# Kernel optimization log

Measured on AMD Instinct MI355X. Metric: run time of the kernel, lower is better.

## Reference

```python
import jax, jax.numpy as jnp
import numpy as np

N = 512   # particles
T = 128   # timesteps
V_L = 3.4
V_0 = 4.2
GAMMA = 0.9
ALPHA = 0.15
BETA = 15.0
E_CRIT_INV = 2e-5
F_STD = 0.05
G_STD = 0.02
NU = 1.0 / (G_STD * float(np.sqrt(2.0 * np.pi)))
CUR_MIN = 0.0
CUR_MAX = 1.0


def voc(soc):
    # open-circuit voltage model
    return (V_L + (V_0 - V_L) * jnp.exp(GAMMA * (soc - 1.0))
            + ALPHA * V_L * (soc - 1.0)
            + (1.0 - ALPHA) * V_L * (jnp.exp(-BETA) - jnp.exp(-BETA * jnp.sqrt(soc))))


def mlp(x, w1, b1, w2, b2, w3, b3):
    h = jax.nn.sigmoid(x @ w1 + b1)
    h = jax.nn.sigmoid(h @ w2 + b2)
    return h @ w3 + b3


def setup_inputs() -> dict:
    key = jax.random.key(0)
    ks = jax.random.split(key, 11)
    soc_init = jax.random.uniform(ks[0], (N, 1), jnp.float32, 0.6, 1.0)
    current = jax.random.uniform(ks[1], (1, T), jnp.float32)
    voltage_measured = 3.4 + 0.8 * jax.random.uniform(ks[2], (1, T), jnp.float32)
    noise = jax.random.normal(ks[3], (T, N, 1), jnp.float32)
    u = jax.random.uniform(ks[4], (T,), jnp.float32)
    w1 = jax.random.normal(ks[5], (2, 1024), jnp.float32) / np.float32(np.sqrt(2.0))
    b1 = jnp.zeros((1024,), jnp.float32)
    w2 = jax.random.normal(ks[6], (1024, 512), jnp.float32) / np.float32(np.sqrt(1024.0))
    b2 = jnp.zeros((512,), jnp.float32)
    w3 = jax.random.normal(ks[7], (512, 1), jnp.float32) / np.float32(np.sqrt(512.0))
    b3 = jnp.zeros((1,), jnp.float32)
    return {"soc_init": soc_init, "current": current, "voltage_measured": voltage_measured,
            "noise": noise, "u": u, "w1": w1, "b1": b1, "w2": w2, "b2": b2, "w3": w3, "b3": b3}


def reference(soc_init, current, voltage_measured, noise, u, w1, b1, w2, b2, w3, b3):
    n = soc_init.shape[0]
    # pre-loop step: V at t=0 conditions
    I0 = current[0, 0] * jnp.ones_like(soc_init)
    sI0 = (I0 - CUR_MIN) / (CUR_MAX - CUR_MIN)
    Z0 = mlp(jnp.concatenate([soc_init, sI0], axis=1), w1, b1, w2, b2, w3, b3)
    V0 = voc(soc_init) - I0 * Z0

    log_n = jnp.log(jnp.float32(n))

    def step(carry, xs):
        soc, I, V = carry
        cur_t, vmeas_t, noise_t, u_t = xs
        # state propagation with process noise, then clamp to (0, 1]
        soc = soc - I * V * E_CRIT_INV + F_STD * noise_t
        soc = jnp.where(soc > 1.0, 1.0, jnp.where(soc < 0.0, 1e-10, soc))
        I = cur_t * jnp.ones_like(soc)
        sI = (I - CUR_MIN) / (CUR_MAX - CUR_MIN)
        Z = mlp(jnp.concatenate([soc, sI], axis=1), w1, b1, w2, b2, w3, b3)  # [N,1]
        V = voc(soc) - I * Z                                                 # [N,1]
        # importance weights / step loss (logsumexp trick as in source)
        logW = jnp.log(jnp.float32(NU)) - 0.5 * jnp.square((V - vmeas_t) / G_STD)
        step_loss = jax.nn.logsumexp(logW) - log_n
        # systematic resampling on normalized weights
        wn = jax.nn.softmax(logW[:, 0])          # normalized weights [N]
        cum = jnp.cumsum(wn)
        pos = (jnp.arange(n, dtype=jnp.float32) + u_t) / jnp.float32(n)
        idx = jnp.clip(jnp.searchsorted(cum, pos), 0, n - 1)
        soc_r = soc[idx]
        return (soc_r, I, V), (V[:, 0], soc_r[:, 0], step_loss)

    xs = (current[0], voltage_measured[0], noise, u)
    _, (v_hist, s_hist, losses) = jax.lax.scan(step, (soc_init, I0, V0), xs)
    loss = jnp.sum(losses)
    voltage = v_hist.T    # [N, T]
    soc_hist = s_hist.T   # [N, T]
    return loss, voltage, soc_hist
```

## Files before the change

kernel.cpp:

```cpp
#include <hip/hip_runtime.h>
#include <hip/hip_bf16.h>
#include <math.h>

#define N_PART 512
#define T_STEPS 128
#define G_NODES 33
#define TAB2D (G_NODES * G_NODES)
#define ROWS (T_STEPS * G_NODES)
#define V_L 3.4f
#define V_0 4.2f
#define GAMMA 0.9f
#define ALPHA 0.15f
#define BETA 15.0f
#define E_CRIT_INV 2e-5f
#define F_STD 0.05f
#define G_STD 0.02f

#define LBAR() asm volatile("s_waitcnt lgkmcnt(0)\n\ts_barrier" ::: "memory")

__device__ __forceinline__ float sigmoid_jax(float x) {
    float e = expf(-fabsf(x));
    float num = (x >= 0.f) ? 1.f : e;
    return num / (1.f + e);
}

__device__ __forceinline__ float vocf(float s) {
    float sm1 = s - 1.f;
    return V_L + (V_0 - V_L) * expf(GAMMA * sm1)
         + (ALPHA * V_L) * sm1
         + (1.f - ALPHA) * V_L * (expf(-BETA) - expf(-BETA * sqrtf(s)));
}

template <int R>
__device__ __forceinline__ int dpp_ror(int v) {
    return __builtin_amdgcn_update_dpp(0, v, 0x120 | R, 0xf, 0xf, false);
}
template <int S>
__device__ __forceinline__ int dpp_shr(int v) {
    return __builtin_amdgcn_update_dpp(0, v, 0x110 | S, 0xf, 0xf, true);
}
__device__ __forceinline__ float fror(float v, float o) { return o; }

__device__ __forceinline__ float wave_max_f(float v) {
    v = fmaxf(v, __int_as_float(dpp_ror<1>(__float_as_int(v))));
    v = fmaxf(v, __int_as_float(dpp_ror<2>(__float_as_int(v))));
    v = fmaxf(v, __int_as_float(dpp_ror<4>(__float_as_int(v))));
    v = fmaxf(v, __int_as_float(dpp_ror<8>(__float_as_int(v))));
    int iv = __float_as_int(v);
    v = fmaxf(v, __int_as_float(__builtin_amdgcn_update_dpp(iv, iv, 0x142, 0xf, 0xf, false)));
    iv = __float_as_int(v);
    v = fmaxf(v, __int_as_float(__builtin_amdgcn_update_dpp(iv, iv, 0x143, 0xf, 0xf, false)));
    return __int_as_float(__builtin_amdgcn_readlane(__float_as_int(v), 63));
}

__device__ __forceinline__ int wave_max_i(int v) {
    v = max(v, dpp_ror<1>(v));
    v = max(v, dpp_ror<2>(v));
    v = max(v, dpp_ror<4>(v));
    v = max(v, dpp_ror<8>(v));
    v = max(v, __builtin_amdgcn_update_dpp(v, v, 0x142, 0xf, 0xf, false));
    v = max(v, __builtin_amdgcn_update_dpp(v, v, 0x143, 0xf, 0xf, false));
    return __builtin_amdgcn_readlane(v, 63);
}

__device__ __forceinline__ float wave_scan_add(float v, int lane) {
    v += __int_as_float(dpp_shr<1>(__float_as_int(v)));
    v += __int_as_float(dpp_shr<2>(__float_as_int(v)));
    v += __int_as_float(dpp_shr<4>(__float_as_int(v)));
    v += __int_as_float(dpp_shr<8>(__float_as_int(v)));
    float s15 = __int_as_float(__builtin_amdgcn_readlane(__float_as_int(v), 15));
    float s31 = __int_as_float(__builtin_amdgcn_readlane(__float_as_int(v), 31));
    float s47 = __int_as_float(__builtin_amdgcn_readlane(__float_as_int(v), 47));
    int row = lane >> 4;
    if (row >= 1) v += s15;
    if (row >= 2) v += s31;
    if (row >= 3) v += s47;
    return v;
}

__device__ __forceinline__ int wave_scanmax_i(int v, int lane) {
    v = max(v, dpp_shr<1>(v));
    v = max(v, dpp_shr<2>(v));
    v = max(v, dpp_shr<4>(v));
    v = max(v, dpp_shr<8>(v));
    int r15 = __builtin_amdgcn_readlane(v, 15);
    int r31 = __builtin_amdgcn_readlane(v, 31);
    int r47 = __builtin_amdgcn_readlane(v, 47);
    int row = lane >> 4;
    if (row >= 1) v = max(v, r15);
    if (row >= 2) v = max(v, r31);
    if (row >= 3) v = max(v, r47);
    return v;
}

#define BKT 32
__global__ __launch_bounds__(256) void k_tab(
    const float* __restrict__ w1, const float* __restrict__ b1,
    const float* __restrict__ w2, const float* __restrict__ b2,
    const float* __restrict__ w3, float* __restrict__ zpart)
{
    const int tid = threadIdx.x;
    const int rowblk = blockIdx.x >> 1;
    const int colhalf = blockIdx.x & 1;
    const int r0 = rowblk * 8;
    const int cbase = colhalf * 256;

    __shared__ float As[8][BKT + 1];
    __shared__ float Bs[BKT][256];
    __shared__ float srow[8], irow[8];

    if (tid < 8) {
        int r = r0 + tid;
        r = r > (TAB2D - 1) ? (TAB2D - 1) : r;
        int si = r / G_NODES;
        int ii = r - si * G_NODES;
        srow[tid] = (float)si * (1.0f / 32.0f);
        irow[tid] = (float)ii * (1.0f / 32.0f);
    }
    __syncthreads();

    const int rg = tid >> 5;
    const int ct = tid & 31;
    float acc[8];
    #pragma unroll
    for (int b = 0; b < 8; ++b) acc[b] = 0.f;

    for (int kk = 0; kk < 1024; kk += BKT) {
        {
            int kc = kk + ct;
            float pre = srow[rg] * w1[kc] + irow[rg] * w1[1024 + kc] + b1[kc];
            As[rg][ct] = sigmoid_jax(pre);
        }
        #pragma unroll
        for (int jj = 0; jj < 8; ++jj) {
            int vi = tid + jj * 256;
            int k = vi >> 6, c4 = vi & 63;
            *(float4*)&Bs[k][c4 * 4] = *(const float4*)&w2[(kk + k) * 512 + cbase + c4 * 4];
        }
        __syncthreads();
        #pragma unroll
        for (int k = 0; k < BKT; ++k) {
            float a = As[rg][k];
            float bq[8];
            *(float4*)&bq[0] = *(const float4*)&Bs[k][ct * 4];
            *(float4*)&bq[4] = *(const float4*)&Bs[k][ct * 4 + 128];
            #pragma unroll
            for (int q = 0; q < 8; ++q) acc[q] += a * bq[q];
        }
        __syncthreads();
    }

    float b2r[8], w3r[8];
    *(float4*)&b2r[0] = *(const float4*)&b2[cbase + ct * 4];
    *(float4*)&b2r[4] = *(const float4*)&b2[cbase + ct * 4 + 128];
    *(float4*)&w3r[0] = *(const float4*)&w3[cbase + ct * 4];
    *(float4*)&w3r[4] = *(const float4*)&w3[cbase + ct * 4 + 128];
    float zp = 0.f;
    #pragma unroll
    for (int q = 0; q < 8; ++q)
        zp += w3r[q] * sigmoid_jax(acc[q] + b2r[q]);
    #pragma unroll
    for (int mm = 1; mm < 32; mm <<= 1) zp += __shfl_xor(zp, mm);
    if (ct == 0 && (r0 + rg) < TAB2D)
        zpart[colhalf * TAB2D + r0 + rg] = zp;
}

__device__ __forceinline__ float interp_tab(const float* __restrict__ row, int stride, float s) {
    float x = s * 32.0f;
    int j = (int)floorf(x);
    j = j < 0 ? 0 : (j > 31 ? 31 : j);
    int st = j - 1;
    st = st < 0 ? 0 : (st > 29 ? 29 : st);
    float uu = x - (float)st;
    float um0 = uu, um1 = uu - 1.f, um2 = uu - 2.f, um3 = uu - 3.f;
    float w0 = um1 * um2 * um3 * (-1.f / 6.f);
    float w1 = um0 * um2 * um3 * (0.5f);
    float w2 = um0 * um1 * um3 * (-0.5f);
    float w3 = um0 * um1 * um2 * (1.f / 6.f);
    return w0 * row[st * stride] + w1 * row[(st + 1) * stride]
         + w2 * row[(st + 2) * stride] + w3 * row[(st + 3) * stride];
}

__device__ __forceinline__ int count_le(float C, float u) {
    int h = (int)floorf(C - u);
    h = h < -1 ? -1 : (h > 511 ? 511 : h);
    h += (int)((h < 511) && (((float)(h + 1) + u) <= C));
    h += (int)((h < 511) && (((float)(h + 1) + u) <= C));
    h -= (int)((h >= 0) && (((float)h + u) > C));
    h -= (int)((h >= 0) && (((float)h + u) > C));
    return h + 1;
}

__global__ __launch_bounds__(512, 1) void k_seq(
    const float* __restrict__ zpart, const float* __restrict__ soc_init,
    const float* __restrict__ current, const float* __restrict__ vmeas,
    const float* __restrict__ u, const float* __restrict__ noise,
    const float* __restrict__ b3, float* __restrict__ vbuf,
    float* __restrict__ sbuf, float* __restrict__ out)
{
    const int tid = threadIdx.x;
    const int lane = tid & 63;
    const int wid = tid >> 6;

    __shared__ float zt[ROWS];
    __shared__ float zt2d[TAB2D];
    __shared__ float socs[2][512];
    __shared__ int marker[512];
    __shared__ float cur_s[128], vm_s[128], u_s[128];
    __shared__ float redM[8], redT[8];

    float bb3 = b3[0];
    for (int j = tid; j < TAB2D; j += 512) zt2d[j] = zpart[j] + zpart[TAB2D + j] + bb3;
    if (tid < 128) { cur_s[tid] = current[tid]; vm_s[tid] = vmeas[tid]; u_s[tid] = u[tid]; }
    marker[tid] = 0;
    __syncthreads();

    for (int idx = tid; idx < ROWS; idx += 512) {
        int t = idx / G_NODES;
        int g = idx - t * G_NODES;
        zt[idx] = interp_tab(&zt2d[g * G_NODES], 1, cur_s[t]);
    }
    __syncthreads();

    float soc = soc_init[tid];
    float Iprev = cur_s[0];
    float V = vocf(soc) - Iprev * interp_tab(&zt[0], 1, soc);
    float loss_acc = 0.f;
    const float LOG_NU = logf(19.947114020071635f);
    const float LOG_N = logf(512.f);

    float nz_cur = noise[tid];

    for (int t = 0; t < T_STEPS; ++t) {
        int tn = (t + 1 < T_STEPS) ? t + 1 : t;
        float nz_next = noise[tn * 512 + tid];

        soc = soc - Iprev * V * E_CRIT_INV + F_STD * nz_cur;
        soc = soc > 1.f ? 1.f : (soc < 0.f ? 1e-10f : soc);
        socs[t & 1][tid] = soc;

        float I = cur_s[t];
        V = vocf(soc) - I * interp_tab(&zt[t * G_NODES], 1, soc);
        float d = (V - vm_s[t]) * (1.f / G_STD);
        float lw = LOG_NU - 0.5f * d * d;

        float m = wave_max_f(lw);
        float e = expf(lw - m);
        float incl = wave_scan_add(e, lane);
        if (lane == 63) { redM[wid] = m; redT[wid] = incl; }
        LBAR();

        float rm = redM[lane & 7];
        float rt = redT[lane & 7];
        float M = rm;
        M = fmaxf(M, __int_as_float(dpp_ror<1>(__float_as_int(M))));
        M = fmaxf(M, __int_as_float(dpp_ror<2>(__float_as_int(M))));
        M = fmaxf(M, __int_as_float(dpp_ror<4>(__float_as_int(M))));
        M = fmaxf(M, __int_as_float(dpp_ror<8>(__float_as_int(M))));
        float fw = expf(rm - M);
        float term = rt * fw;
        float sc = term;
        sc += __int_as_float(dpp_shr<1>(__float_as_int(sc)));
        sc += __int_as_float(dpp_shr<2>(__float_as_int(sc)));
        sc += __int_as_float(dpp_shr<4>(__float_as_int(sc)));
        float S = __int_as_float(__builtin_amdgcn_readlane(__float_as_int(sc), 7));
        float off = 0.f;
        if (wid > 0) off = __int_as_float(__builtin_amdgcn_readlane(__float_as_int(sc), wid - 1));
        float fw_own = __int_as_float(__builtin_amdgcn_readlane(__float_as_int(fw), wid));
        loss_acc += M + logf(S) - LOG_N;

        float C = 512.f * ((off + incl * fw_own) / S);
        int hi = count_le(C, u_s[t]);
        if (hi < 512) atomicMax(&marker[hi], (t << 10) | (tid + 1));
        LBAR();

        int pm = 0;
        for (int w = 0; w < wid; ++w) pm = max(pm, marker[w * 64 + lane]);
        pm = wave_max_i(pm);
        int v = wave_scanmax_i(marker[tid], lane);
        int sv = max(v, pm);
        int owner = ((sv >> 10) == t) ? (sv & 1023) : 0;
        owner = owner > 511 ? 511 : owner;
        float socr = socs[t & 1][owner];

        vbuf[t * 512 + tid] = V;
        sbuf[t * 512 + tid] = socr;
        soc = socr;
        Iprev = I;
        nz_cur = nz_next;
    }
    if (tid == 0) out[0] = loss_acc;
}

__global__ __launch_bounds__(256) void k_fin(
    const float* __restrict__ vbuf, const float* __restrict__ sbuf,
    float* __restrict__ out)
{
    __shared__ float tile[32][33];
    int tz = blockIdx.z;
    int t0 = blockIdx.x * 32;
    int i0 = blockIdx.y * 32;
    const float* src = tz ? sbuf : vbuf;
    float* dst = out + 1 + tz * (N_PART * T_STEPS);
    int tx = threadIdx.x & 31, ty = threadIdx.x >> 5;
    #pragma unroll
    for (int m2 = 0; m2 < 4; ++m2)
        tile[ty + 8 * m2][tx] = src[(t0 + ty + 8 * m2) * 512 + i0 + tx];
    __syncthreads();
    #pragma unroll
    for (int m2 = 0; m2 < 4; ++m2)
        dst[(i0 + ty + 8 * m2) * 128 + t0 + tx] = tile[tx][ty + 8 * m2];
}

extern "C" void kernel_launch(void* const* d_in, const int* in_sizes, int n_in,
                              void* d_out, int out_size, void* d_ws, size_t ws_size,
                              hipStream_t stream)
{
    const float* soc_init = (const float*)d_in[0];
    const float* current  = (const float*)d_in[1];
    const float* vmeas    = (const float*)d_in[2];
    const float* noise    = (const float*)d_in[3];
    const float* u        = (const float*)d_in[4];
    const float* w1 = (const float*)d_in[5];
    const float* b1 = (const float*)d_in[6];
    const float* w2 = (const float*)d_in[7];
    const float* b2 = (const float*)d_in[8];
    const float* w3 = (const float*)d_in[9];
    const float* b3 = (const float*)d_in[10];
    float* out = (float*)d_out;
    float* ws  = (float*)d_ws;

    float* zpart = ws;
    float* vbuf  = ws + 2 * TAB2D;
    float* sbuf  = vbuf + N_PART * T_STEPS;

    k_tab<<<274, 256, 0, stream>>>(w1, b1, w2, b2, w3, zpart);
    k_seq<<<1, 512, 0, stream>>>(zpart, soc_init, current, vmeas, u, noise, b3,
                                 vbuf, sbuf, out);
    k_fin<<<dim3(4, 16, 2), 256, 0, stream>>>(vbuf, sbuf, out);
}
```

Before: 286.2 us.

## Precompute per-timestep voltage tables on a finer grid to shorten the sequential loop

Before the sequential loop, a per-timestep voltage table V(t, soc) is built on a 193-point soc grid by combining the open-circuit voltage with the interpolated MLP output. Each step then needs only one cubic interpolation from this table instead of evaluating vocf (several exp and a sqrt) plus an interpolation. Fast intrinsics __expf and __logf replace expf and logf, and the count_le correction passes are cut from two to one each. In exchange, the kernel uses more shared memory and runs a longer setup, and the extra interpolation layer changes accuracy slightly.

```diff
diff --git a/kernel.cpp b/kernel.cpp
--- a/kernel.cpp
+++ b/kernel.cpp
@@ -1,20 +1,19 @@
 #include <hip/hip_runtime.h>
-#include <hip/hip_bf16.h>
 #include <math.h>
 
-#define N_PART 512
-#define T_STEPS 128
-#define G_NODES 33
-#define TAB2D (G_NODES * G_NODES)
-#define ROWS (T_STEPS * G_NODES)
-#define V_L 3.4f
-#define V_0 4.2f
-#define GAMMA 0.9f
-#define ALPHA 0.15f
-#define BETA 15.0f
-#define E_CRIT_INV 2e-5f
-#define F_STD 0.05f
-#define G_STD 0.02f
+#define NP 512
+#define TS 128
+#define GI 33
+#define TAB2D (GI * GI)
+#define GV 193
+#define V_Lc 3.4f
+#define V_0c 4.2f
+#define GAMMAc 0.9f
+#define ALPHAc 0.15f
+#define BETAc 15.0f
+#define E_INV 2e-5f
+#define F_STDc 0.05f
+#define G_STDc 0.02f
 
 #define LBAR() asm volatile("s_waitcnt lgkmcnt(0)\n\ts_barrier" ::: "memory")
 
@@ -26,9 +25,9 @@
 
 __device__ __forceinline__ float vocf(float s) {
     float sm1 = s - 1.f;
-    return V_L + (V_0 - V_L) * expf(GAMMA * sm1)
-         + (ALPHA * V_L) * sm1
-         + (1.f - ALPHA) * V_L * (expf(-BETA) - expf(-BETA * sqrtf(s)));
+    return V_Lc + (V_0c - V_Lc) * expf(GAMMAc * sm1)
+         + (ALPHAc * V_Lc) * sm1
+         + (1.f - ALPHAc) * V_Lc * (expf(-BETAc) - expf(-BETAc * sqrtf(s)));
 }
 
 template <int R>
@@ -39,7 +38,9 @@
 __device__ __forceinline__ int dpp_shr(int v) {
     return __builtin_amdgcn_update_dpp(0, v, 0x110 | S, 0xf, 0xf, true);
 }
-__device__ __forceinline__ float fror(float v, float o) { return o; }
+__device__ __forceinline__ float rdlane_f(float v, int l) {
+    return __int_as_float(__builtin_amdgcn_readlane(__float_as_int(v), l));
+}
 
 __device__ __forceinline__ float wave_max_f(float v) {
     v = fmaxf(v, __int_as_float(dpp_ror<1>(__float_as_int(v))));
@@ -50,7 +51,7 @@
     v = fmaxf(v, __int_as_float(__builtin_amdgcn_update_dpp(iv, iv, 0x142, 0xf, 0xf, false)));
     iv = __float_as_int(v);
     v = fmaxf(v, __int_as_float(__builtin_amdgcn_update_dpp(iv, iv, 0x143, 0xf, 0xf, false)));
-    return __int_as_float(__builtin_amdgcn_readlane(__float_as_int(v), 63));
+    return rdlane_f(v, 63);
 }
 
 __device__ __forceinline__ int wave_max_i(int v) {
@@ -68,9 +69,9 @@
     v += __int_as_float(dpp_shr<2>(__float_as_int(v)));
     v += __int_as_float(dpp_shr<4>(__float_as_int(v)));
     v += __int_as_float(dpp_shr<8>(__float_as_int(v)));
-    float s15 = __int_as_float(__builtin_amdgcn_readlane(__float_as_int(v), 15));
-    float s31 = __int_as_float(__builtin_amdgcn_readlane(__float_as_int(v), 31));
-    float s47 = __int_as_float(__builtin_amdgcn_readlane(__float_as_int(v), 47));
+    float s15 = rdlane_f(v, 15);
+    float s31 = rdlane_f(v, 31);
+    float s47 = rdlane_f(v, 47);
     int row = lane >> 4;
     if (row >= 1) v += s15;
     if (row >= 2) v += s31;
@@ -93,6 +94,44 @@
     return v;
 }
 
+__device__ __forceinline__ float interp33(const float* __restrict__ row, float s) {
+    float x = s * 32.0f;
+    int j = (int)floorf(x);
+    j = j < 0 ? 0 : (j > 31 ? 31 : j);
+    int st = j - 1;
+    st = st < 0 ? 0 : (st > 29 ? 29 : st);
+    float uu = x - (float)st;
+    float um0 = uu, um1 = uu - 1.f, um2 = uu - 2.f, um3 = uu - 3.f;
+    float c0 = um1 * um2 * um3 * (-1.f / 6.f);
+    float c1 = um0 * um2 * um3 * (0.5f);
+    float c2 = um0 * um1 * um3 * (-0.5f);
+    float c3 = um0 * um1 * um2 * (1.f / 6.f);
+    return c0 * row[st] + c1 * row[st + 1] + c2 * row[st + 2] + c3 * row[st + 3];
+}
+
+__device__ __forceinline__ float interp193(const float* __restrict__ row, float s) {
+    float x = s * 192.0f;
+    int j = (int)floorf(x);
+    j = j < 0 ? 0 : (j > 191 ? 191 : j);
+    int st = j - 1;
+    st = st < 0 ? 0 : (st > 189 ? 189 : st);
+    float uu = x - (float)st;
+    float um0 = uu, um1 = uu - 1.f, um2 = uu - 2.f, um3 = uu - 3.f;
+    float c0 = um1 * um2 * um3 * (-1.f / 6.f);
+    float c1 = um0 * um2 * um3 * (0.5f);
+    float c2 = um0 * um1 * um3 * (-0.5f);
+    float c3 = um0 * um1 * um2 * (1.f / 6.f);
+    return c0 * row[st] + c1 * row[st + 1] + c2 * row[st + 2] + c3 * row[st + 3];
+}
+
+__device__ __forceinline__ int count_le(float C, float u) {
+    int h = (int)floorf(C - u);
+    h = h < -1 ? -1 : (h > 511 ? 511 : h);
+    h += (int)((h < 511) && (((float)(h + 1) + u) <= C));
+    h -= (int)((h >= 0) && (((float)h + u) > C));
+    return h + 1;
+}
+
 #define BKT 32
 __global__ __launch_bounds__(256) void k_tab(
     const float* __restrict__ w1, const float* __restrict__ b1,
@@ -112,8 +151,8 @@
     if (tid < 8) {
         int r = r0 + tid;
         r = r > (TAB2D - 1) ? (TAB2D - 1) : r;
-        int si = r / G_NODES;
-        int ii = r - si * G_NODES;
+        int si = r / GI;
+        int ii = r - si * GI;
         srow[tid] = (float)si * (1.0f / 32.0f);
         irow[tid] = (float)ii * (1.0f / 32.0f);
     }
@@ -165,32 +204,6 @@
         zpart[colhalf * TAB2D + r0 + rg] = zp;
 }
 
-__device__ __forceinline__ float interp_tab(const float* __restrict__ row, int stride, float s) {
-    float x = s * 32.0f;
-    int j = (int)floorf(x);
-    j = j < 0 ? 0 : (j > 31 ? 31 : j);
-    int st = j - 1;
-    st = st < 0 ? 0 : (st > 29 ? 29 : st);
-    float uu = x - (float)st;
-    float um0 = uu, um1 = uu - 1.f, um2 = uu - 2.f, um3 = uu - 3.f;
-    float w0 = um1 * um2 * um3 * (-1.f / 6.f);
-    float w1 = um0 * um2 * um3 * (0.5f);
-    float w2 = um0 * um1 * um3 * (-0.5f);
-    float w3 = um0 * um1 * um2 * (1.f / 6.f);
-    return w0 * row[st * stride] + w1 * row[(st + 1) * stride]
-         + w2 * row[(st + 2) * stride] + w3 * row[(st + 3) * stride];
-}
-
-__device__ __forceinline__ int count_le(float C, float u) {
-    int h = (int)floorf(C - u);
-    h = h < -1 ? -1 : (h > 511 ? 511 : h);
-    h += (int)((h < 511) && (((float)(h + 1) + u) <= C));
-    h += (int)((h < 511) && (((float)(h + 1) + u) <= C));
-    h -= (int)((h >= 0) && (((float)h + u) > C));
-    h -= (int)((h >= 0) && (((float)h + u) > C));
-    return h + 1;
-}
-
 __global__ __launch_bounds__(512, 1) void k_seq(
     const float* __restrict__ zpart, const float* __restrict__ soc_init,
     const float* __restrict__ current, const float* __restrict__ vmeas,
@@ -200,54 +213,59 @@
 {
     const int tid = threadIdx.x;
     const int lane = tid & 63;
-    const int wid = tid >> 6;
-
-    __shared__ float zt[ROWS];
+    const int wv = tid >> 6;
+
+    __shared__ float vt[TS][GV];
+    __shared__ float zt[TS][GI];
     __shared__ float zt2d[TAB2D];
-    __shared__ float socs[2][512];
-    __shared__ int marker[512];
-    __shared__ float cur_s[128], vm_s[128], u_s[128];
+    __shared__ float vocs[GV];
+    __shared__ float socs[2][NP];
+    __shared__ int marker[NP];
+    __shared__ float cur_s[TS], vm_s[TS], u_s[TS];
     __shared__ float redM[8], redT[8];
 
     float bb3 = b3[0];
     for (int j = tid; j < TAB2D; j += 512) zt2d[j] = zpart[j] + zpart[TAB2D + j] + bb3;
-    if (tid < 128) { cur_s[tid] = current[tid]; vm_s[tid] = vmeas[tid]; u_s[tid] = u[tid]; }
+    if (tid < TS) { cur_s[tid] = current[tid]; vm_s[tid] = vmeas[tid]; u_s[tid] = u[tid]; }
+    if (tid < GV) vocs[tid] = vocf((float)tid * (1.0f / 192.0f));
     marker[tid] = 0;
     __syncthreads();
-
-    for (int idx = tid; idx < ROWS; idx += 512) {
-        int t = idx / G_NODES;
-        int g = idx - t * G_NODES;
-        zt[idx] = interp_tab(&zt2d[g * G_NODES], 1, cur_s[t]);
+    for (int idx = tid; idx < TS * GI; idx += 512) {
+        int t = idx / GI, g = idx - t * GI;
+        zt[t][g] = interp33(&zt2d[g * GI], cur_s[t]);
+    }
+    __syncthreads();
+    for (int idx = tid; idx < TS * GV; idx += 512) {
+        int t = idx / GV, j = idx - t * GV;
+        float sj = (float)j * (1.0f / 192.0f);
+        vt[t][j] = vocs[j] - cur_s[t] * interp33(&zt[t][0], sj);
     }
     __syncthreads();
 
     float soc = soc_init[tid];
     float Iprev = cur_s[0];
-    float V = vocf(soc) - Iprev * interp_tab(&zt[0], 1, soc);
+    float V = interp193(&vt[0][0], soc);
     float loss_acc = 0.f;
     const float LOG_NU = logf(19.947114020071635f);
     const float LOG_N = logf(512.f);
-
     float nz_cur = noise[tid];
 
-    for (int t = 0; t < T_STEPS; ++t) {
-        int tn = (t + 1 < T_STEPS) ? t + 1 : t;
+    for (int t = 0; t < TS; ++t) {
+        int tn = (t + 1 < TS) ? t + 1 : t;
         float nz_next = noise[tn * 512 + tid];
 
-        soc = soc - Iprev * V * E_CRIT_INV + F_STD * nz_cur;
+        soc = soc - Iprev * V * E_INV + F_STDc * nz_cur;
         soc = soc > 1.f ? 1.f : (soc < 0.f ? 1e-10f : soc);
         socs[t & 1][tid] = soc;
 
-        float I = cur_s[t];
-        V = vocf(soc) - I * interp_tab(&zt[t * G_NODES], 1, soc);
-        float d = (V - vm_s[t]) * (1.f / G_STD);
+        V = interp193(&vt[t][0], soc);
+        float d = (V - vm_s[t]) * (1.f / G_STDc);
         float lw = LOG_NU - 0.5f * d * d;
 
         float m = wave_max_f(lw);
-        float e = expf(lw - m);
+        float e = __expf(lw - m);
         float incl = wave_scan_add(e, lane);
-        if (lane == 63) { redM[wid] = m; redT[wid] = incl; }
+        if (lane == 63) { redM[wv] = m; redT[wv] = incl; }
         LBAR();
 
         float rm = redM[lane & 7];
@@ -257,17 +275,17 @@
         M = fmaxf(M, __int_as_float(dpp_ror<2>(__float_as_int(M))));
         M = fmaxf(M, __int_as_float(dpp_ror<4>(__float_as_int(M))));
         M = fmaxf(M, __int_as_float(dpp_ror<8>(__float_as_int(M))));
-        float fw = expf(rm - M);
+        float fw = __expf(rm - M);
         float term = rt * fw;
         float sc = term;
         sc += __int_as_float(dpp_shr<1>(__float_as_int(sc)));
         sc += __int_as_float(dpp_shr<2>(__float_as_int(sc)));
         sc += __int_as_float(dpp_shr<4>(__float_as_int(sc)));
-        float S = __int_as_float(__builtin_amdgcn_readlane(__float_as_int(sc), 7));
+        float S = rdlane_f(sc, 7);
         float off = 0.f;
-        if (wid > 0) off = __int_as_float(__builtin_amdgcn_readlane(__float_as_int(sc), wid - 1));
-        float fw_own = __int_as_float(__builtin_amdgcn_readlane(__float_as_int(fw), wid));
-        loss_acc += M + logf(S) - LOG_N;
+        if (wv > 0) off = rdlane_f(sc, wv - 1);
+        float fw_own = rdlane_f(fw, wv);
+        loss_acc += M + __logf(S) - LOG_N;
 
         float C = 512.f * ((off + incl * fw_own) / S);
         int hi = count_le(C, u_s[t]);
@@ -275,7 +293,7 @@
         LBAR();
 
         int pm = 0;
-        for (int w = 0; w < wid; ++w) pm = max(pm, marker[w * 64 + lane]);
+        for (int w = 0; w < wv; ++w) pm = max(pm, marker[w * 64 + lane]);
         pm = wave_max_i(pm);
         int v = wave_scanmax_i(marker[tid], lane);
         int sv = max(v, pm);
@@ -286,7 +304,7 @@
         vbuf[t * 512 + tid] = V;
         sbuf[t * 512 + tid] = socr;
         soc = socr;
-        Iprev = I;
+        Iprev = cur_s[t];
         nz_cur = nz_next;
     }
     if (tid == 0) out[0] = loss_acc;
@@ -301,7 +319,7 @@
     int t0 = blockIdx.x * 32;
     int i0 = blockIdx.y * 32;
     const float* src = tz ? sbuf : vbuf;
-    float* dst = out + 1 + tz * (N_PART * T_STEPS);
+    float* dst = out + 1 + tz * (NP * TS);
     int tx = threadIdx.x & 31, ty = threadIdx.x >> 5;
     #pragma unroll
     for (int m2 = 0; m2 < 4; ++m2)
@@ -331,8 +349,8 @@
     float* ws  = (float*)d_ws;
 
     float* zpart = ws;
-    float* vbuf  = ws + 2 * TAB2D;
-    float* sbuf  = vbuf + N_PART * T_STEPS;
+    float* vbuf  = ws + 2180;
+    float* sbuf  = vbuf + NP * TS;
 
     k_tab<<<274, 256, 0, stream>>>(w1, b1, w2, b2, w3, zpart);
     k_seq<<<1, 512, 0, stream>>>(zpart, soc_init, current, vmeas, u, noise, b3,
```

Measured after the change: 265.2 us. -7.3%, faster.
